# Performance work log

Hardware: AMD Instinct MI355X
Metric: run time of the kernel (lower is better)

Reference implementation:

```python
import jax, jax.numpy as jnp
import numpy as np

B, NX, NC, D, H = 2, 512, 4096, 1024, 16
HD = D // H  # head_dim = context_dim // heads
LN_EPS = 1e-5


def setup_inputs() -> dict:
    key = jax.random.key(0)
    k0, k1, k2, k3, k4 = jax.random.split(key, 5)
    x = jax.random.normal(k0, (B, NX, D), dtype=jnp.float32)
    c = jax.random.normal(k1, (B, NC, D), dtype=jnp.float32)
    attn_mask = jax.random.randint(k2, (B, NX, NC), 0, 2).astype(bool)
    # learned params
    ln_w = jnp.ones((D,), jnp.float32)
    ln_b = jnp.zeros((D,), jnp.float32)
    Wq = jax.random.normal(k3, (D, D), dtype=jnp.float32) * 0.02  # to_q (query_dim -> inner_dim)
    Wo = jax.random.normal(k4, (D, D), dtype=jnp.float32) * 0.02  # to_out (inner_dim -> query_dim)
    return {"x": x, "c": c, "attn_mask": attn_mask, "ln_w": ln_w, "ln_b": ln_b, "Wq": Wq, "Wo": Wo}


def _layernorm(x, w, b):
    mu = jnp.mean(x, axis=-1, keepdims=True)
    var = jnp.mean(jnp.square(x - mu), axis=-1, keepdims=True)
    return (x - mu) * jax.lax.rsqrt(var + LN_EPS) * w + b


def reference(x, c, attn_mask, ln_w, ln_b, Wq, Wo):
    scale = HD ** (-0.5)
    xn = _layernorm(x, ln_w, ln_b)
    q = (xn @ Wq).reshape(B, NX, H, HD).transpose(0, 2, 1, 3)      # (B,H,NX,HD)
    kv0 = c.reshape(B, NC, H, HD).transpose(0, 2, 1, 3)             # (B,H,NC,HD) -- kvt=(kv0,kv0)
    kv = jnp.concatenate([q, kv0], axis=2)                          # kv_append_q=True -> (B,H,NX+NC,HD)
    # mask: ones for the appended-q block, user mask for context block
    m = jnp.broadcast_to(attn_mask[:, None, :, :], (B, H, NX, NC))
    full_mask = jnp.concatenate([jnp.ones((B, H, NX, NX), bool), m], axis=-1)
    sim = jnp.einsum('bhqd,bhkd->bhqk', q * scale, kv)              # (B,H,NX,NX+NC)
    neg = -jnp.finfo(sim.dtype).max
    sim = jnp.where(full_mask, sim, neg)
    attn = jax.nn.softmax(sim, axis=-1)
    a = jnp.einsum('bhqk,bhkd->bhqd', attn, kv)
    o = a.transpose(0, 2, 1, 3).reshape(B, NX, H * HD) @ Wo
    return (o, kv0)
```

## Files before the change

### kernel.cpp

```cpp
#include <hip/hip_runtime.h>

#define B_  2
#define NX_ 512
#define NC_ 4096
#define D_  1024
#define H_  16
#define HD_ 64
#define NT_ (NX_ + NC_)
#define NSPLIT 4
#define KBS (NT_ / 64 / NSPLIT)

typedef float  floatx4  __attribute__((ext_vector_type(4)));
typedef __bf16 bf16x8   __attribute__((ext_vector_type(8)));
typedef unsigned short ushort8v __attribute__((ext_vector_type(8)));

__device__ __forceinline__ bf16x8 as_bf16x8(ushort8v u) {
    union { ushort8v u; bf16x8 b; } c; c.u = u; return c.b;
}
__device__ __forceinline__ unsigned short f2bf(float f) {
    unsigned u = __float_as_uint(f);
    u += 0x7FFF + ((u >> 16) & 1);
    return (unsigned short)(u >> 16);
}
__device__ __forceinline__ bf16x8 cvt8(float4 a, float4 b, float s) {
    ushort8v u;
    u[0] = f2bf(a.x * s); u[1] = f2bf(a.y * s); u[2] = f2bf(a.z * s); u[3] = f2bf(a.w * s);
    u[4] = f2bf(b.x * s); u[5] = f2bf(b.y * s); u[6] = f2bf(b.z * s); u[7] = f2bf(b.w * s);
    return as_bf16x8(u);
}

__global__ __launch_bounds__(256)
void prep_kernel(const float* __restrict__ x, const float* __restrict__ lw,
                 const float* __restrict__ lb, const float* __restrict__ Wq,
                 const float* __restrict__ Wo, const int* __restrict__ mask,
                 const float* __restrict__ c,
                 unsigned short* __restrict__ xnb, unsigned short* __restrict__ WqT,
                 unsigned short* __restrict__ WoT, unsigned* __restrict__ bits,
                 unsigned short* __restrict__ cbf, float* __restrict__ gz,
                 float* __restrict__ kv0o) {
    int blk = blockIdx.x;
    int tid = threadIdx.x;
    if (blk < 1024) {
        int row = blk;
        float4 v = reinterpret_cast<const float4*>(x)[(size_t)row * (D_ / 4) + tid];
        float s  = v.x + v.y + v.z + v.w;
        float s2 = v.x * v.x + v.y * v.y + v.z * v.z + v.w * v.w;
        #pragma unroll
        for (int off = 32; off > 0; off >>= 1) {
            s  += __shfl_down(s, off);
            s2 += __shfl_down(s2, off);
        }
        __shared__ float sm[4], sm2[4], stat[2];
        int wv = tid >> 6;
        if ((tid & 63) == 0) { sm[wv] = s; sm2[wv] = s2; }
        __syncthreads();
        if (tid == 0) {
            float S  = sm[0] + sm[1] + sm[2] + sm[3];
            float S2 = sm2[0] + sm2[1] + sm2[2] + sm2[3];
            float mu  = S * (1.0f / D_);
            float var = fmaxf(S2 * (1.0f / D_) - mu * mu, 0.0f);
            stat[0] = mu;
            stat[1] = rsqrtf(var + 1e-5f);
        }
        __syncthreads();
        float mu = stat[0], rs = stat[1];
        float4 w4 = reinterpret_cast<const float4*>(lw)[tid];
        float4 b4 = reinterpret_cast<const float4*>(lb)[tid];
        ushort4 o;
        o.x = f2bf((v.x - mu) * rs * w4.x + b4.x);
        o.y = f2bf((v.y - mu) * rs * w4.y + b4.y);
        o.z = f2bf((v.z - mu) * rs * w4.z + b4.z);
        o.w = f2bf((v.w - mu) * rs * w4.w + b4.w);
        reinterpret_cast<ushort4*>(xnb)[(size_t)row * (D_ / 4) + tid] = o;
    } else if (blk < 1536) {
        int which = (blk - 1024) >> 8;
        int t = (blk - 1024) & 255;
        const float* W = which ? Wo : Wq;
        unsigned short* WT = which ? WoT : WqT;
        __shared__ unsigned short T[64][72];
        int row0 = (t >> 4) * 64, col0 = (t & 15) * 64;
        int r = tid >> 2, ch = (tid & 3) * 16;
        const float* src = W + (size_t)(row0 + r) * D_ + col0 + ch;
        unsigned short vals[16];
        #pragma unroll
        for (int k = 0; k < 4; ++k) {
            float4 v = reinterpret_cast<const float4*>(src)[k];
            vals[k*4+0] = f2bf(v.x); vals[k*4+1] = f2bf(v.y);
            vals[k*4+2] = f2bf(v.z); vals[k*4+3] = f2bf(v.w);
        }
        #pragma unroll
        for (int i = 0; i < 16; ++i) T[ch + i][r] = vals[i];
        __syncthreads();
        unsigned short* dst = WT + (size_t)(col0 + r) * D_ + row0 + ch;
        uint4 o0 = *reinterpret_cast<uint4*>(&T[r][ch]);
        uint4 o1 = *reinterpret_cast<uint4*>(&T[r][ch + 8]);
        *reinterpret_cast<uint4*>(dst)     = o0;
        *reinterpret_cast<uint4*>(dst + 8) = o1;
    } else if (blk < 2048) {
        size_t w = (size_t)(blk - 1536) * 256 + tid;
        const int* src = mask + w * 32;
        unsigned b = 0;
        #pragma unroll
        for (int k = 0; k < 8; ++k) {
            int4 v = reinterpret_cast<const int4*>(src)[k];
            b |= (v.x != 0 ? 1u : 0u) << (k * 4 + 0);
            b |= (v.y != 0 ? 1u : 0u) << (k * 4 + 1);
            b |= (v.z != 0 ? 1u : 0u) << (k * 4 + 2);
            b |= (v.w != 0 ? 1u : 0u) << (k * 4 + 3);
        }
        bits[w] = b;
    } else if (blk < 10240) {
        size_t i = ((size_t)(blk - 2048) * 256 + tid) * 4;
        float4 v = *reinterpret_cast<const float4*>(c + i);
        ushort4 o;
        o.x = f2bf(v.x); o.y = f2bf(v.y); o.z = f2bf(v.z); o.w = f2bf(v.w);
        *reinterpret_cast<ushort4*>(cbf + i) = o;
        if (kv0o != nullptr) {
            size_t row = i >> 10;
            int dd = (int)(i & 1023);
            int hh = dd >> 6, d4 = (dd & 63) >> 2;
            int bb = (int)(row >> 12);
            int n  = (int)(row & 4095);
            size_t o4 = (((size_t)(bb * 16 + hh) * NC_ + n) << 4) + d4;
            reinterpret_cast<float4*>(kv0o)[o4] = v;
        }
    } else {
        size_t i = ((size_t)(blk - 10240) * 256 + tid) * 4;
        float4 z = {0.f, 0.f, 0.f, 0.f};
        *reinterpret_cast<float4*>(gz + i) = z;
    }
}

__global__ __launch_bounds__(256)
void kv0_kernel(const float* __restrict__ c, float* __restrict__ out2) {
    size_t i = (size_t)blockIdx.x * 256 + threadIdx.x;
    int d4 = (int)(i & 15);
    size_t r = i >> 4;
    int n = (int)(r % NC_);
    size_t r2 = r / NC_;
    int h = (int)(r2 & (H_ - 1));
    int b = (int)(r2 >> 4);
    float4 v = *reinterpret_cast<const float4*>(c + ((size_t)(b * NC_ + n)) * D_ + h * HD_ + d4 * 4);
    reinterpret_cast<float4*>(out2)[i] = v;
}

__global__ __launch_bounds__(256)
void gemm_bt_kernel(const unsigned short* __restrict__ A, const unsigned short* __restrict__ BT,
                    unsigned short* __restrict__ Cb) {
    int tid = threadIdx.x;
    int lane = tid & 63, wave = tid >> 6;
    int m16 = lane & 15, g = lane >> 4, g8 = g * 8;
    int row0 = blockIdx.y * 64, col0 = blockIdx.x * 32;

    const unsigned short* arow  = A  + (size_t)(row0 + 16 * wave + m16) * D_ + g8;
    const unsigned short* brow0 = BT + (size_t)(col0 + m16)            * D_ + g8;
    const unsigned short* brow1 = BT + (size_t)(col0 + 16 + m16)       * D_ + g8;

    floatx4 acc0 = (floatx4){0.f, 0.f, 0.f, 0.f};
    floatx4 acc1 = (floatx4){0.f, 0.f, 0.f, 0.f};

    #pragma unroll 4
    for (int kc = 0; kc < 16; ++kc) {
        int k0 = kc * 64;
        bf16x8 fa0 = as_bf16x8(*reinterpret_cast<const ushort8v*>(arow  + k0));
        bf16x8 fa1 = as_bf16x8(*reinterpret_cast<const ushort8v*>(arow  + k0 + 32));
        bf16x8 f00 = as_bf16x8(*reinterpret_cast<const ushort8v*>(brow0 + k0));
        bf16x8 f01 = as_bf16x8(*reinterpret_cast<const ushort8v*>(brow0 + k0 + 32));
        bf16x8 f10 = as_bf16x8(*reinterpret_cast<const ushort8v*>(brow1 + k0));
        bf16x8 f11 = as_bf16x8(*reinterpret_cast<const ushort8v*>(brow1 + k0 + 32));
        acc0 = __builtin_amdgcn_mfma_f32_16x16x32_bf16(fa0, f00, acc0, 0, 0, 0);
        acc0 = __builtin_amdgcn_mfma_f32_16x16x32_bf16(fa1, f01, acc0, 0, 0, 0);
        acc1 = __builtin_amdgcn_mfma_f32_16x16x32_bf16(fa0, f10, acc1, 0, 0, 0);
        acc1 = __builtin_amdgcn_mfma_f32_16x16x32_bf16(fa1, f11, acc1, 0, 0, 0);
    }
    #pragma unroll
    for (int reg = 0; reg < 4; ++reg) {
        size_t rr = (size_t)(row0 + 16 * wave + g * 4 + reg) * D_ + col0;
        Cb[rr + m16]      = f2bf(acc0[reg]);
        Cb[rr + 16 + m16] = f2bf(acc1[reg]);
    }
}

__global__ __launch_bounds__(256)
void gemm_attn_kernel(const float* __restrict__ gacc, const float* __restrict__ gacc_l,
                      const unsigned short* __restrict__ BT, float* __restrict__ out) {
    int tid = threadIdx.x;
    int lane = tid & 63, wave = tid >> 6;
    int m16 = lane & 15, g = lane >> 4, g8 = g * 8;
    int row0 = blockIdx.y * 64, col0 = blockIdx.x * 32;
    int row = row0 + 16 * wave + m16;

    const float* arow = gacc + (size_t)row * D_ + g8;
    const float* lrow = gacc_l + (size_t)row * H_;
    const unsigned short* brow0 = BT + (size_t)(col0 + m16)      * D_ + g8;
    const unsigned short* brow1 = BT + (size_t)(col0 + 16 + m16) * D_ + g8;

    floatx4 acc0 = (floatx4){0.f, 0.f, 0.f, 0.f};
    floatx4 acc1 = (floatx4){0.f, 0.f, 0.f, 0.f};

    #pragma unroll 4
    for (int kc = 0; kc < 16; ++kc) {
        int k0 = kc * 64;
        float inv = 1.0f / fmaxf(lrow[kc], 1e-35f);
        float4 a0 = *reinterpret_cast<const float4*>(arow + k0);
        float4 a1 = *reinterpret_cast<const float4*>(arow + k0 + 4);
        float4 a2 = *reinterpret_cast<const float4*>(arow + k0 + 32);
        float4 a3 = *reinterpret_cast<const float4*>(arow + k0 + 36);
        bf16x8 fa0 = cvt8(a0, a1, inv);
        bf16x8 fa1 = cvt8(a2, a3, inv);
        bf16x8 f00 = as_bf16x8(*reinterpret_cast<const ushort8v*>(brow0 + k0));
        bf16x8 f01 = as_bf16x8(*reinterpret_cast<const ushort8v*>(brow0 + k0 + 32));
        bf16x8 f10 = as_bf16x8(*reinterpret_cast<const ushort8v*>(brow1 + k0));
        bf16x8 f11 = as_bf16x8(*reinterpret_cast<const ushort8v*>(brow1 + k0 + 32));
        acc0 = __builtin_amdgcn_mfma_f32_16x16x32_bf16(fa0, f00, acc0, 0, 0, 0);
        acc0 = __builtin_amdgcn_mfma_f32_16x16x32_bf16(fa1, f01, acc0, 0, 0, 0);
        acc1 = __builtin_amdgcn_mfma_f32_16x16x32_bf16(fa0, f10, acc1, 0, 0, 0);
        acc1 = __builtin_amdgcn_mfma_f32_16x16x32_bf16(fa1, f11, acc1, 0, 0, 0);
    }
    #pragma unroll
    for (int reg = 0; reg < 4; ++reg) {
        size_t rr = (size_t)(row0 + 16 * wave + g * 4 + reg) * D_ + col0;
        out[rr + m16]      = acc0[reg];
        out[rr + 16 + m16] = acc1[reg];
    }
}

__global__ __launch_bounds__(256, 4)
void attn_kernel(const unsigned short* __restrict__ qbf,
                 const unsigned short* __restrict__ cbf,
                 const unsigned* __restrict__ maskbits,
                 float* __restrict__ gacc, float* __restrict__ gacc_l) {
    int blk   = blockIdx.x;
    int bh    = ((blk >> 8) << 3) | (blk & 7);
    int inner = (blk >> 3) & 31;
    int qt    = inner & 7;
    int split = inner >> 3;
    int h  = bh & 15;
    int b  = bh >> 4;
    int tid  = threadIdx.x;
    int lane = tid & 63;
    int wave = tid >> 6;
    int m16  = lane & 15;
    int g    = lane >> 4;
    int g8   = g * 8;

    __shared__ unsigned short Ks [64][72];
    __shared__ unsigned short Kts[64][72];
    __shared__ unsigned short Ps [64][64];

    const unsigned short* qrow = qbf + ((size_t)(b * NX_ + qt * 64 + 16 * wave + m16)) * D_ + h * HD_;
    bf16x8 qa0 = as_bf16x8(*reinterpret_cast<const ushort8v*>(qrow + g8));
    bf16x8 qa1 = as_bf16x8(*reinterpret_cast<const ushort8v*>(qrow + 32 + g8));

    floatx4 acc_o[4];
    #pragma unroll
    for (int td = 0; td < 4; ++td) acc_o[td] = (floatx4){0.f, 0.f, 0.f, 0.f};
    floatx4 acc_l = (floatx4){0.f, 0.f, 0.f, 0.f};

    ushort8v ones_u;
    #pragma unroll
    for (int j = 0; j < 8; ++j) ones_u[j] = 0x3F80;
    bf16x8 onesf = as_bf16x8(ones_u);

    int Kg = tid >> 4;
    int Dg = tid & 15;
    int pcst = ((Kg >> 1) + (Dg >> 1)) & 7;
    int prsw = 2 * ((m16 >> 2) & 3);

    int kb0 = split * KBS;

    uint2 rows[4];
    {
        const unsigned short* s0 = (kb0 < 8)
            ? qbf + ((size_t)(b * NX_ + kb0 * 64 + 4 * Kg)) * D_ + h * HD_ + 4 * Dg
            : cbf + ((size_t)(b * NC_ + kb0 * 64 - NX_ + 4 * Kg)) * D_ + h * HD_ + 4 * Dg;
        #pragma unroll
        for (int kk = 0; kk < 4; ++kk)
            rows[kk] = *reinterpret_cast<const uint2*>(s0 + (size_t)kk * D_);
    }

    for (int i = 0; i < KBS; ++i) {
        int kb = kb0 + i;
        __syncthreads();

        unsigned mw0[4], mw1[4];
        if (kb >= 8) {
            #pragma unroll
            for (int r = 0; r < 4; ++r) {
                size_t mi = ((size_t)(b * NX_ + qt * 64 + 16 * wave + g * 4 + r)) * (NC_ / 32)
                          + (size_t)(kb - 8) * 2;
                uint2 w = *reinterpret_cast<const uint2*>(&maskbits[mi]);
                mw0[r] = w.x; mw1[r] = w.y;
            }
        }

        #pragma unroll
        for (int kk = 0; kk < 4; ++kk)
            *reinterpret_cast<uint2*>(&Ks[4 * Kg + kk][4 * Dg]) = rows[kk];
        #pragma unroll
        for (int i2 = 0; i2 < 4; ++i2) {
            unsigned sel = (i2 & 1) ? 0x07060302u : 0x05040100u;
            unsigned r0 = (i2 >> 1) ? rows[0].y : rows[0].x;
            unsigned r1 = (i2 >> 1) ? rows[1].y : rows[1].x;
            unsigned r2 = (i2 >> 1) ? rows[2].y : rows[2].x;
            unsigned r3 = (i2 >> 1) ? rows[3].y : rows[3].x;
            uint2 cw;
            cw.x = __builtin_amdgcn_perm(r1, r0, sel);
            cw.y = __builtin_amdgcn_perm(r3, r2, sel);
            *reinterpret_cast<uint2*>(&Kts[4 * Dg + i2][pcst * 8 + 4 * (Kg & 1)]) = cw;
        }

        {
            int kbn = (i + 1 < KBS) ? kb + 1 : kb;
            const unsigned short* sn = (kbn < 8)
                ? qbf + ((size_t)(b * NX_ + kbn * 64 + 4 * Kg)) * D_ + h * HD_ + 4 * Dg
                : cbf + ((size_t)(b * NC_ + kbn * 64 - NX_ + 4 * Kg)) * D_ + h * HD_ + 4 * Dg;
            #pragma unroll
            for (int kk = 0; kk < 4; ++kk)
                rows[kk] = *reinterpret_cast<const uint2*>(sn + (size_t)kk * D_);
        }

        asm volatile("s_waitcnt lgkmcnt(0)" ::: "memory");
        __builtin_amdgcn_s_barrier();
        __builtin_amdgcn_sched_barrier(0);
        asm volatile("" ::: "memory");

        floatx4 accs[4];
        #pragma unroll
        for (int t = 0; t < 4; ++t) {
            bf16x8 b0 = as_bf16x8(*reinterpret_cast<ushort8v*>(&Ks[16 * t + m16][g8]));
            bf16x8 b1 = as_bf16x8(*reinterpret_cast<ushort8v*>(&Ks[16 * t + m16][32 + g8]));
            floatx4 d = (floatx4){0.f, 0.f, 0.f, 0.f};
            d = __builtin_amdgcn_mfma_f32_16x16x32_bf16(qa0, b0, d, 0, 0, 0);
            d = __builtin_amdgcn_mfma_f32_16x16x32_bf16(qa1, b1, d, 0, 0, 0);
            accs[t] = d;
        }

        const float C1 = 0.18033688011112042f;
        const float C2 = 92.33248261689366f;
        #pragma unroll
        for (int t = 0; t < 4; ++t) {
            int cc = 2 * t + (m16 >> 3);
            #pragma unroll
            for (int r = 0; r < 4; ++r) {
                float e = fminf(fmaf(accs[t][r], C1, -C2), 0.0f);
                float p = __builtin_amdgcn_exp2f(e);
                if (kb >= 8) {
                    unsigned w = (t < 2) ? mw0[r] : mw1[r];
                    unsigned bit = (w >> ((16 * t + m16) & 31)) & 1u;
                    p = bit ? p : 0.0f;
                }
                int prow = 16 * wave + g * 4 + r;
                int pc = (cc + 2 * g) & 7;
                Ps[prow][pc * 8 + (m16 & 7)] = (unsigned short)(__float_as_uint(p) >> 16);
            }
        }
        asm volatile("s_waitcnt lgkmcnt(0)" ::: "memory");

        bf16x8 p0 = as_bf16x8(*reinterpret_cast<ushort8v*>(&Ps[16 * wave + m16][((g + prsw) & 7) * 8]));
        bf16x8 p1 = as_bf16x8(*reinterpret_cast<ushort8v*>(&Ps[16 * wave + m16][((4 + g + prsw) & 7) * 8]));
        acc_l = __builtin_amdgcn_mfma_f32_16x16x32_bf16(p0, onesf, acc_l, 0, 0, 0);
        acc_l = __builtin_amdgcn_mfma_f32_16x16x32_bf16(p1, onesf, acc_l, 0, 0, 0);
        #pragma unroll
        for (int td = 0; td < 4; ++td) {
            int row = 16 * td + m16;
            int rh = row >> 3;
            bf16x8 v0 = as_bf16x8(*reinterpret_cast<ushort8v*>(&Kts[row][((g + rh) & 7) * 8]));
            bf16x8 v1 = as_bf16x8(*reinterpret_cast<ushort8v*>(&Kts[row][((4 + g + rh) & 7) * 8]));
            acc_o[td] = __builtin_amdgcn_mfma_f32_16x16x32_bf16(p0, v0, acc_o[td], 0, 0, 0);
            acc_o[td] = __builtin_amdgcn_mfma_f32_16x16x32_bf16(p1, v1, acc_o[td], 0, 0, 0);
        }
    }

    #pragma unroll
    for (int r = 0; r < 4; ++r) {
        int qrow_ = qt * 64 + 16 * wave + g * 4 + r;
        float* dst = gacc + ((size_t)(b * NX_ + qrow_)) * D_ + h * HD_;
        #pragma unroll
        for (int td = 0; td < 4; ++td)
            unsafeAtomicAdd(&dst[16 * td + m16], acc_o[td][r]);
        if (m16 == 0)
            unsafeAtomicAdd(&gacc_l[(size_t)(b * NX_ + qrow_) * H_ + h], acc_l[r]);
    }
}

extern "C" void kernel_launch(void* const* d_in, const int* in_sizes, int n_in,
                              void* d_out, int out_size, void* d_ws, size_t ws_size,
                              hipStream_t stream) {
    (void)in_sizes; (void)n_in; (void)out_size;
    const float* x    = (const float*)d_in[0];
    const float* c    = (const float*)d_in[1];
    const int*   mask = (const int*)d_in[2];
    const float* ln_w = (const float*)d_in[3];
    const float* ln_b = (const float*)d_in[4];
    const float* Wq   = (const float*)d_in[5];
    const float* Wo   = (const float*)d_in[6];
    float* out  = (float*)d_out;
    float* out2 = out + (size_t)B_ * NX_ * D_;

    const size_t SCRATCH_FLOATS = 8011776;
    bool use_ws = (d_ws != nullptr) && (ws_size >= SCRATCH_FLOATS * sizeof(float));
    float* base = use_ws ? (float*)d_ws : out2;

    unsigned short* qbf      = (unsigned short*)(base);
    unsigned*       maskbits = (unsigned*)(base + 524288);
    float*          gacc     = base + 655360;
    float*          gacc_l   = base + 1703936;
    unsigned short* WqT      = (unsigned short*)(base + 1720320);
    unsigned short* WoT      = (unsigned short*)(base + 2244608);
    unsigned short* xnb      = (unsigned short*)(base + 2768896);
    unsigned short* cbf      = (unsigned short*)(base + 3817472);

    prep_kernel<<<11280, 256, 0, stream>>>(x, ln_w, ln_b, Wq, Wo, mask, c,
                                           xnb, WqT, WoT, maskbits, cbf, gacc,
                                           use_ws ? out2 : nullptr);
    gemm_bt_kernel<<<dim3(32, 16), 256, 0, stream>>>(xnb, WqT, qbf);
    attn_kernel<<<NSPLIT * 256, 256, 0, stream>>>(qbf, cbf, maskbits, gacc, gacc_l);
    gemm_attn_kernel<<<dim3(32, 16), 256, 0, stream>>>(gacc, gacc_l, WoT, out);
    if (!use_ws)
        kv0_kernel<<<(B_ * H_ * NC_ * HD_ / 4) / 256, 256, 0, stream>>>(c, out2);
}
```

Measured before the change: 213.8 us.

## Stage B tiles through LDS and software-prefetch operands in projection GEMMs

In both projection GEMMs, each wave used to load the full 32-column B tile from global memory on its own. Now the block loads each B tile once, cooperatively, into a padded LDS buffer, and every wave reads its fragments from there. The next k-chunk's A and B operands are loaded into registers before the current chunk's MFMAs run, giving a register-level double buffer. This trades redundant global and L2 traffic for two block barriers per k-step and a single LDS buffer.

Measured after the change: 191.9 us. -10.2%, faster.

```diff
diff --git a/kernel.cpp b/kernel.cpp
--- a/kernel.cpp
+++ b/kernel.cpp
@@ -147,27 +147,43 @@
 __global__ __launch_bounds__(256)
 void gemm_bt_kernel(const unsigned short* __restrict__ A, const unsigned short* __restrict__ BT,
                     unsigned short* __restrict__ Cb) {
+    __shared__ unsigned short Bs[32][72];
     int tid = threadIdx.x;
     int lane = tid & 63, wave = tid >> 6;
     int m16 = lane & 15, g = lane >> 4, g8 = g * 8;
     int row0 = blockIdx.y * 64, col0 = blockIdx.x * 32;
+    int rB = tid >> 3, chB = (tid & 7) * 8;
 
     const unsigned short* arow  = A  + (size_t)(row0 + 16 * wave + m16) * D_ + g8;
-    const unsigned short* brow0 = BT + (size_t)(col0 + m16)            * D_ + g8;
-    const unsigned short* brow1 = BT + (size_t)(col0 + 16 + m16)       * D_ + g8;
+    const unsigned short* bbase = BT + (size_t)(col0 + rB) * D_ + chB;
 
     floatx4 acc0 = (floatx4){0.f, 0.f, 0.f, 0.f};
     floatx4 acc1 = (floatx4){0.f, 0.f, 0.f, 0.f};
 
-    #pragma unroll 4
+    ushort8v a0r = *reinterpret_cast<const ushort8v*>(arow);
+    ushort8v a1r = *reinterpret_cast<const ushort8v*>(arow + 32);
+    uint4    b0  = *reinterpret_cast<const uint4*>(bbase);
+
     for (int kc = 0; kc < 16; ++kc) {
-        int k0 = kc * 64;
-        bf16x8 fa0 = as_bf16x8(*reinterpret_cast<const ushort8v*>(arow  + k0));
-        bf16x8 fa1 = as_bf16x8(*reinterpret_cast<const ushort8v*>(arow  + k0 + 32));
-        bf16x8 f00 = as_bf16x8(*reinterpret_cast<const ushort8v*>(brow0 + k0));
-        bf16x8 f01 = as_bf16x8(*reinterpret_cast<const ushort8v*>(brow0 + k0 + 32));
-        bf16x8 f10 = as_bf16x8(*reinterpret_cast<const ushort8v*>(brow1 + k0));
-        bf16x8 f11 = as_bf16x8(*reinterpret_cast<const ushort8v*>(brow1 + k0 + 32));
+        if (kc) {
+            asm volatile("s_waitcnt lgkmcnt(0)" ::: "memory");
+            __builtin_amdgcn_s_barrier();
+        }
+        *reinterpret_cast<uint4*>(&Bs[rB][chB]) = b0;
+        bf16x8 fa0 = as_bf16x8(a0r);
+        bf16x8 fa1 = as_bf16x8(a1r);
+        if (kc < 15) {
+            int k0 = (kc + 1) * 64;
+            a0r = *reinterpret_cast<const ushort8v*>(arow + k0);
+            a1r = *reinterpret_cast<const ushort8v*>(arow + k0 + 32);
+            b0  = *reinterpret_cast<const uint4*>(bbase + k0);
+        }
+        asm volatile("s_waitcnt lgkmcnt(0)" ::: "memory");
+        __builtin_amdgcn_s_barrier();
+        bf16x8 f00 = as_bf16x8(*reinterpret_cast<ushort8v*>(&Bs[m16][g8]));
+        bf16x8 f01 = as_bf16x8(*reinterpret_cast<ushort8v*>(&Bs[m16][32 + g8]));
+        bf16x8 f10 = as_bf16x8(*reinterpret_cast<ushort8v*>(&Bs[16 + m16][g8]));
+        bf16x8 f11 = as_bf16x8(*reinterpret_cast<ushort8v*>(&Bs[16 + m16][32 + g8]));
         acc0 = __builtin_amdgcn_mfma_f32_16x16x32_bf16(fa0, f00, acc0, 0, 0, 0);
         acc0 = __builtin_amdgcn_mfma_f32_16x16x32_bf16(fa1, f01, acc0, 0, 0, 0);
         acc1 = __builtin_amdgcn_mfma_f32_16x16x32_bf16(fa0, f10, acc1, 0, 0, 0);
@@ -184,34 +200,52 @@
 __global__ __launch_bounds__(256)
 void gemm_attn_kernel(const float* __restrict__ gacc, const float* __restrict__ gacc_l,
                       const unsigned short* __restrict__ BT, float* __restrict__ out) {
+    __shared__ unsigned short Bs[32][72];
     int tid = threadIdx.x;
     int lane = tid & 63, wave = tid >> 6;
     int m16 = lane & 15, g = lane >> 4, g8 = g * 8;
     int row0 = blockIdx.y * 64, col0 = blockIdx.x * 32;
+    int rB = tid >> 3, chB = (tid & 7) * 8;
     int row = row0 + 16 * wave + m16;
 
     const float* arow = gacc + (size_t)row * D_ + g8;
     const float* lrow = gacc_l + (size_t)row * H_;
-    const unsigned short* brow0 = BT + (size_t)(col0 + m16)      * D_ + g8;
-    const unsigned short* brow1 = BT + (size_t)(col0 + 16 + m16) * D_ + g8;
+    const unsigned short* bbase = BT + (size_t)(col0 + rB) * D_ + chB;
 
     floatx4 acc0 = (floatx4){0.f, 0.f, 0.f, 0.f};
     floatx4 acc1 = (floatx4){0.f, 0.f, 0.f, 0.f};
 
-    #pragma unroll 4
+    float4 pa0 = *reinterpret_cast<const float4*>(arow);
+    float4 pa1 = *reinterpret_cast<const float4*>(arow + 4);
+    float4 pa2 = *reinterpret_cast<const float4*>(arow + 32);
+    float4 pa3 = *reinterpret_cast<const float4*>(arow + 36);
+    float  pl  = lrow[0];
+    uint4  b0  = *reinterpret_cast<const uint4*>(bbase);
+
     for (int kc = 0; kc < 16; ++kc) {
-        int k0 = kc * 64;
-        float inv = 1.0f / fmaxf(lrow[kc], 1e-35f);
-        float4 a0 = *reinterpret_cast<const float4*>(arow + k0);
-        float4 a1 = *reinterpret_cast<const float4*>(arow + k0 + 4);
-        float4 a2 = *reinterpret_cast<const float4*>(arow + k0 + 32);
-        float4 a3 = *reinterpret_cast<const float4*>(arow + k0 + 36);
-        bf16x8 fa0 = cvt8(a0, a1, inv);
-        bf16x8 fa1 = cvt8(a2, a3, inv);
-        bf16x8 f00 = as_bf16x8(*reinterpret_cast<const ushort8v*>(brow0 + k0));
-        bf16x8 f01 = as_bf16x8(*reinterpret_cast<const ushort8v*>(brow0 + k0 + 32));
-        bf16x8 f10 = as_bf16x8(*reinterpret_cast<const ushort8v*>(brow1 + k0));
-        bf16x8 f11 = as_bf16x8(*reinterpret_cast<const ushort8v*>(brow1 + k0 + 32));
+        if (kc) {
+            asm volatile("s_waitcnt lgkmcnt(0)" ::: "memory");
+            __builtin_amdgcn_s_barrier();
+        }
+        *reinterpret_cast<uint4*>(&Bs[rB][chB]) = b0;
+        float inv = 1.0f / fmaxf(pl, 1e-35f);
+        bf16x8 fa0 = cvt8(pa0, pa1, inv);
+        bf16x8 fa1 = cvt8(pa2, pa3, inv);
+        if (kc < 15) {
+            int k0 = (kc + 1) * 64;
+            pa0 = *reinterpret_cast<const float4*>(arow + k0);
+            pa1 = *reinterpret_cast<const float4*>(arow + k0 + 4);
+            pa2 = *reinterpret_cast<const float4*>(arow + k0 + 32);
+            pa3 = *reinterpret_cast<const float4*>(arow + k0 + 36);
+            pl  = lrow[kc + 1];
+            b0  = *reinterpret_cast<const uint4*>(bbase + k0);
+        }
+        asm volatile("s_waitcnt lgkmcnt(0)" ::: "memory");
+        __builtin_amdgcn_s_barrier();
+        bf16x8 f00 = as_bf16x8(*reinterpret_cast<ushort8v*>(&Bs[m16][g8]));
+        bf16x8 f01 = as_bf16x8(*reinterpret_cast<ushort8v*>(&Bs[m16][32 + g8]));
+        bf16x8 f10 = as_bf16x8(*reinterpret_cast<ushort8v*>(&Bs[16 + m16][g8]));
+        bf16x8 f11 = as_bf16x8(*reinterpret_cast<ushort8v*>(&Bs[16 + m16][32 + g8]));
         acc0 = __builtin_amdgcn_mfma_f32_16x16x32_bf16(fa0, f00, acc0, 0, 0, 0);
         acc0 = __builtin_amdgcn_mfma_f32_16x16x32_bf16(fa1, f01, acc0, 0, 0, 0);
         acc1 = __builtin_amdgcn_mfma_f32_16x16x32_bf16(fa0, f10, acc1, 0, 0, 0);
```
